# Performance work log

Measured on AMD Instinct MI355X. Metric: run time of the kernel, lower is better.

## Reference

```python
import jax, jax.numpy as jnp
import numpy as np

TOP_K = 2


def setup_inputs() -> dict:
    key = jax.random.key(0)
    k0, k1, k2, k3 = jax.random.split(key, 4)
    T, H, E, I = 512, 2048, 16, 1024  # tokens, hidden, experts, intermediate
    return {
        "hidden_states": jax.random.normal(k0, (T, H), jnp.float32),
        "router_weight": jax.random.normal(k1, (E, H), jnp.float32) * 0.02,
        "w13": jax.random.normal(k2, (E, H, 2 * I), jnp.float32) * 0.02,  # fused gate+up
        "w2": jax.random.normal(k3, (E, I, H), jnp.float32) * 0.02,        # down proj
    }


def reference(hidden_states, router_weight, w13, w2):
    x = hidden_states                                   # [T, H]
    E = router_weight.shape[0]
    # Router: linear (no bias) -> softmax -> top-k -> renormalize
    logits = x @ router_weight.T                        # [T, E]
    probs = jax.nn.softmax(logits, axis=-1)
    vals, idx = jax.lax.top_k(probs, TOP_K)             # [T, K]
    vals = vals / jnp.sum(vals, axis=-1, keepdims=True)
    # Dense combine weights [T, E]: zero except the top-k experts per token
    cw = jnp.sum(jax.nn.one_hot(idx, E, dtype=x.dtype) * vals[..., None], axis=1)
    # Scan over experts; each expert runs a SwiGLU MLP over all tokens,
    # scaled by its (mostly-zero) combine weight. Keeps peak memory at [T, I].
    def body(acc, params):
        w13_e, w2_e, cw_e = params                      # [H,2I], [I,H], [T]
        g, u = jnp.split(x @ w13_e, 2, axis=-1)         # [T, I] each
        acc = acc + cw_e[:, None] * ((jax.nn.silu(g) * u) @ w2_e)
        return acc, None
    out, _ = jax.lax.scan(body, jnp.zeros_like(x), (w13, w2, cw.T))
    return out
```

## Files before the change

### kernel.cpp

```cpp
#include <hip/hip_runtime.h>

#define T_TOK 512
#define HID   2048
#define NEXP  16
#define IDIM  1024
#define KC    64

typedef __attribute__((ext_vector_type(8))) short bf16x8;
typedef __attribute__((ext_vector_type(4))) float f32x4;
typedef __attribute__((ext_vector_type(4))) float float4v;

__device__ __forceinline__ unsigned short f2bf(float f) {
    union { float f; unsigned u; } v; v.f = f;
    return (unsigned short)((v.u + 0x7FFFu + ((v.u >> 16) & 1u)) >> 16);
}

__device__ __forceinline__ unsigned pack2(float lo, float hi) {
    return (unsigned)f2bf(lo) | ((unsigned)f2bf(hi) << 16);
}

__device__ __forceinline__ bf16x8 pack8(const float* s) {
    bf16x8 r;
#pragma unroll
    for (int i = 0; i < 8; ++i) r[i] = (short)f2bf(s[i]);
    return r;
}

__global__ __launch_bounds__(256) void router_kernel(
    const float* __restrict__ x, const float* __restrict__ rw,
    int* __restrict__ cnt, int* __restrict__ tok,
    int* __restrict__ rowid, float* __restrict__ wt,
    unsigned short* __restrict__ xb)
{
    int t = blockIdx.x;
    int tid = threadIdx.x;
    const float* xr = x + (size_t)t * HID;

    {
        int c = tid * 8;
        float4v a = *(const float4v*)(xr + c);
        float4v b = *(const float4v*)(xr + c + 4);
        float tmp[8];
#pragma unroll
        for (int i = 0; i < 4; ++i) { tmp[i] = a[i]; tmp[4 + i] = b[i]; }
        *(bf16x8*)(xb + (size_t)t * HID + c) = pack8(tmp);
    }

    float acc[NEXP];
#pragma unroll
    for (int e = 0; e < NEXP; ++e) acc[e] = 0.f;

    for (int k = tid; k < HID; k += 256) {
        float xv = xr[k];
#pragma unroll
        for (int e = 0; e < NEXP; ++e) acc[e] += xv * rw[e * HID + k];
    }

    __shared__ float red[4][NEXP];
    int lane = tid & 63, wv = tid >> 6;
#pragma unroll
    for (int e = 0; e < NEXP; ++e) {
        float v = acc[e];
#pragma unroll
        for (int off = 32; off > 0; off >>= 1) v += __shfl_down(v, off);
        if (lane == 0) red[wv][e] = v;
    }
    __syncthreads();

    if (tid == 0) {
        float l[NEXP];
        float mx = -1e30f;
#pragma unroll
        for (int e = 0; e < NEXP; ++e) {
            l[e] = red[0][e] + red[1][e] + red[2][e] + red[3][e];
            mx = fmaxf(mx, l[e]);
        }
        float s = 0.f;
#pragma unroll
        for (int e = 0; e < NEXP; ++e) { l[e] = __expf(l[e] - mx); s += l[e]; }
        float inv_s = 1.f / s;
        int i0 = 0; float v0 = -1.f;
        int i1 = 0; float v1 = -2.f;
#pragma unroll
        for (int e = 0; e < NEXP; ++e) {
            float p = l[e] * inv_s;
            if (p > v0)      { v1 = v0; i1 = i0; v0 = p; i0 = e; }
            else if (p > v1) { v1 = p; i1 = e; }
        }
        float inv = 1.f / (v0 + v1);
        int p0 = atomicAdd(&cnt[i0], 1);
        tok[i0 * T_TOK + p0] = t; rowid[i0 * T_TOK + p0] = 2 * t;     wt[i0 * T_TOK + p0] = v0 * inv;
        int p1 = atomicAdd(&cnt[i1], 1);
        tok[i1 * T_TOK + p1] = t; rowid[i1 * T_TOK + p1] = 2 * t + 1; wt[i1 * T_TOK + p1] = v1 * inv;
    }
}

#define LOADW(buf, kk_, stride_) { \
    buf[0] = *(const float4v*)(wsrc + (size_t)((kk_) + kg * 2)     * (stride_)); \
    buf[1] = *(const float4v*)(wsrc + (size_t)((kk_) + kg * 2 + 1) * (stride_)); }

#define STOREW(buf) { _Pragma("unroll") \
    for (int j2 = 0; j2 < 4; ++j2) { \
        int colw = cg * 4 + j2; \
        *(unsigned*)((char*)Ws + ((colw * 128 + kg * 4) ^ ((colw & 7) << 4))) = \
            pack2(buf[0][j2], buf[1][j2]); } }

#define LOADX(buf, kk_) { \
    buf[0] = *(const bf16x8*)(xsrc + (kk_)); \
    buf[1] = *(const bf16x8*)(xsrc + (kk_) + 8); }

#define STOREX(buf) { \
    *(bf16x8*)((char*)Xs + ((xrow * 128 + xq * 32)      ^ xswz)) = buf[0]; \
    *(bf16x8*)((char*)Xs + ((xrow * 128 + xq * 32 + 16) ^ xswz)) = buf[1]; }

__global__ __launch_bounds__(512, 4) void gemm1_kernel(
    const unsigned short* __restrict__ xb, const float* __restrict__ w13,
    const int* __restrict__ cnt, const int* __restrict__ tok,
    const int* __restrict__ rowid, const float* __restrict__ wt,
    unsigned short* __restrict__ h)
{
    int bid = blockIdx.x;
    int e  = bid >> 5;
    int c0 = (bid & 31) * 32;
    int n = cnt[e];
    int tid = threadIdx.x;

    __shared__ __align__(16) short Xs[128 * KC];
    __shared__ __align__(16) short Ws[64 * KC];
    __shared__ int   tks[128];
    __shared__ int   rws[128];
    __shared__ float wts[128];

    const float* wbase = w13 + (size_t)e * HID * (2 * IDIM);

    int cg = tid & 15, kg = tid >> 4;
    const float* wsrc = wbase + ((cg < 8) ? (c0 + cg * 4)
                                          : (IDIM + c0 + (cg - 8) * 4));
    int xrow = tid >> 2, xq = tid & 3;
    int xswz = (xrow & 7) << 4;

    int wave = tid >> 6, lane = tid & 63;
    int lr = lane & 15, lh = lane >> 4;
    int swzA = (lr & 7) << 4;

    for (int t0 = 0; t0 < n; t0 += 128) {
        int nt = min(128, n - t0);
        __syncthreads();
        if (tid < 128) {
            int idx = t0 + min(tid, nt - 1);
            tks[tid] = tok[e * T_TOK + idx];
            rws[tid] = rowid[e * T_TOK + idx];
            wts[tid] = wt[e * T_TOK + idx];
        }
        __syncthreads();

        const unsigned short* xsrc = xb + (size_t)tks[xrow] * HID + xq * 16;

        f32x4 accG[2], accU[2];
#pragma unroll
        for (int i = 0; i < 2; ++i) { accG[i] = (f32x4)0.f; accU[i] = (f32x4)0.f; }

        float4v wbufA[2], wbufB[2];
        bf16x8 xbufA[2], xbufB[2];
        LOADW(wbufA, 0, 2 * IDIM); LOADX(xbufA, 0);

#define G1_MFMA() { \
        if (wave * 16 < nt) { _Pragma("unroll") \
            for (int s = 0; s < 2; ++s) { \
                int kb = (s * 32 + lh * 8) * 2; \
                bf16x8 a = *(const bf16x8*)((char*)Xs + (((wave * 16 + lr) * 128 + kb) ^ swzA)); \
                _Pragma("unroll") for (int cf = 0; cf < 2; ++cf) { \
                    int colg = cf * 16 + lr; \
                    bf16x8 bg = *(const bf16x8*)((char*)Ws + ((colg * 128 + kb) ^ swzA)); \
                    accG[cf] = __builtin_amdgcn_mfma_f32_16x16x32_bf16(a, bg, accG[cf], 0, 0, 0); \
                    bf16x8 bu = *(const bf16x8*)((char*)Ws + (((32 + colg) * 128 + kb) ^ swzA)); \
                    accU[cf] = __builtin_amdgcn_mfma_f32_16x16x32_bf16(a, bu, accU[cf], 0, 0, 0); \
                } \
            } \
        } }

        for (int kk = 0; kk < HID; kk += 2 * KC) {
            LOADW(wbufB, kk + KC, 2 * IDIM); LOADX(xbufB, kk + KC);
            STOREW(wbufA); STOREX(xbufA);
            __syncthreads();
            G1_MFMA();
            __syncthreads();
            if (kk + 2 * KC < HID) { LOADW(wbufA, kk + 2 * KC, 2 * IDIM); LOADX(xbufA, kk + 2 * KC); }
            STOREW(wbufB); STOREX(xbufB);
            __syncthreads();
            G1_MFMA();
            __syncthreads();
        }

#pragma unroll
        for (int cf = 0; cf < 2; ++cf)
#pragma unroll
            for (int r = 0; r < 4; ++r) {
                int row = wave * 16 + lh * 4 + r;
                if (row < nt) {
                    float g = accG[cf][r], u = accU[cf][r];
                    float sg = g / (1.f + __expf(-g));
                    float v = wts[row] * sg * u;
                    h[(size_t)rws[row] * IDIM + c0 + cf * 16 + lr] = f2bf(v);
                }
            }
    }
}

__global__ __launch_bounds__(512, 4) void gemm2_kernel(
    const unsigned short* __restrict__ h, const float* __restrict__ w2,
    const int* __restrict__ cnt, const int* __restrict__ tok,
    const int* __restrict__ rowid,
    float* __restrict__ out)
{
    int bid = blockIdx.x;
    int e  = bid >> 5;
    int c0 = (bid & 31) * 64;
    int n = cnt[e];
    int tid = threadIdx.x;

    __shared__ __align__(16) short Xs[128 * KC];
    __shared__ __align__(16) short Ws[64 * KC];
    __shared__ int   tks[128];
    __shared__ int   rws[128];

    const float* wbase = w2 + (size_t)e * IDIM * HID;

    int cg = tid & 15, kg = tid >> 4;
    const float* wsrc = wbase + c0 + cg * 4;
    int xrow = tid >> 2, xq = tid & 3;
    int xswz = (xrow & 7) << 4;

    int wave = tid >> 6, lane = tid & 63;
    int lr = lane & 15, lh = lane >> 4;
    int swzA = (lr & 7) << 4;

    for (int t0 = 0; t0 < n; t0 += 128) {
        int nt = min(128, n - t0);
        __syncthreads();
        if (tid < 128) {
            int idx = t0 + min(tid, nt - 1);
            tks[tid] = tok[e * T_TOK + idx];
            rws[tid] = rowid[e * T_TOK + idx];
        }
        __syncthreads();

        const unsigned short* xsrc = h + (size_t)rws[xrow] * IDIM + xq * 16;

        f32x4 acc[4];
#pragma unroll
        for (int i = 0; i < 4; ++i) acc[i] = (f32x4)0.f;

        float4v wbufA[2], wbufB[2];
        bf16x8 xbufA[2], xbufB[2];
        LOADW(wbufA, 0, HID); LOADX(xbufA, 0);

#define G2_MFMA() { \
        if (wave * 16 < nt) { _Pragma("unroll") \
            for (int s = 0; s < 2; ++s) { \
                int kb = (s * 32 + lh * 8) * 2; \
                bf16x8 a = *(const bf16x8*)((char*)Xs + (((wave * 16 + lr) * 128 + kb) ^ swzA)); \
                _Pragma("unroll") for (int cf = 0; cf < 4; ++cf) { \
                    int col = cf * 16 + lr; \
                    bf16x8 b = *(const bf16x8*)((char*)Ws + ((col * 128 + kb) ^ swzA)); \
                    acc[cf] = __builtin_amdgcn_mfma_f32_16x16x32_bf16(a, b, acc[cf], 0, 0, 0); \
                } \
            } \
        } }

        for (int kk = 0; kk < IDIM; kk += 2 * KC) {
            LOADW(wbufB, kk + KC, HID); LOADX(xbufB, kk + KC);
            STOREW(wbufA); STOREX(xbufA);
            __syncthreads();
            G2_MFMA();
            __syncthreads();
            if (kk + 2 * KC < IDIM) { LOADW(wbufA, kk + 2 * KC, HID); LOADX(xbufA, kk + 2 * KC); }
            STOREW(wbufB); STOREX(xbufB);
            __syncthreads();
            G2_MFMA();
            __syncthreads();
        }

#pragma unroll
        for (int cf = 0; cf < 4; ++cf)
#pragma unroll
            for (int r = 0; r < 4; ++r) {
                int row = wave * 16 + lh * 4 + r;
                if (row < nt)
                    atomicAdd(&out[(size_t)tks[row] * HID + c0 + cf * 16 + lr], acc[cf][r]);
            }
    }
}

extern "C" void kernel_launch(void* const* d_in, const int* in_sizes, int n_in,
                              void* d_out, int out_size, void* d_ws, size_t ws_size,
                              hipStream_t stream) {
    const float* x   = (const float*)d_in[0];
    const float* rw  = (const float*)d_in[1];
    const float* w13 = (const float*)d_in[2];
    const float* w2  = (const float*)d_in[3];
    float* out = (float*)d_out;

    int* cnt   = (int*)d_ws;
    int* tok   = cnt + 64;
    int* rowid = tok + NEXP * T_TOK;
    float* wt  = (float*)(rowid + NEXP * T_TOK);
    unsigned short* h  = (unsigned short*)((char*)d_ws + 131072);
    unsigned short* xb = (unsigned short*)((char*)d_ws + 131072 + 2097152);

    hipMemsetAsync(out, 0, (size_t)T_TOK * HID * sizeof(float), stream);
    hipMemsetAsync(cnt, 0, 64 * sizeof(int), stream);

    router_kernel<<<T_TOK, 256, 0, stream>>>(x, rw, cnt, tok, rowid, wt, xb);
    gemm1_kernel<<<512, 512, 0, stream>>>(xb, w13, cnt, tok, rowid, wt, h);
    gemm2_kernel<<<512, 512, 0, stream>>>(h, w2, cnt, tok, rowid, out);
}
```

Before: 133.2 us.

## Double-buffer LDS tiles to halve barriers in both MoE GEMM kernels

Both grouped GEMM kernels now keep two LDS buffers for the X and W tiles. The next tile is written into the alternate buffer while MFMAs read the current one, so each K-step needs one barrier instead of two. The aim is less barrier stall and better overlap of the LDS stores with compute. In exchange, LDS use per block doubles (about 48KB), which may cut the number of resident blocks below the launch-bounds target of 4.

```diff
diff --git a/kernel.cpp b/kernel.cpp
--- a/kernel.cpp
+++ b/kernel.cpp
@@ -99,19 +99,19 @@
     buf[0] = *(const float4v*)(wsrc + (size_t)((kk_) + kg * 2)     * (stride_)); \
     buf[1] = *(const float4v*)(wsrc + (size_t)((kk_) + kg * 2 + 1) * (stride_)); }
 
-#define STOREW(buf) { _Pragma("unroll") \
+#define STOREW(buf, Wd) { _Pragma("unroll") \
     for (int j2 = 0; j2 < 4; ++j2) { \
         int colw = cg * 4 + j2; \
-        *(unsigned*)((char*)Ws + ((colw * 128 + kg * 4) ^ ((colw & 7) << 4))) = \
+        *(unsigned*)((char*)(Wd) + ((colw * 128 + kg * 4) ^ ((colw & 7) << 4))) = \
             pack2(buf[0][j2], buf[1][j2]); } }
 
 #define LOADX(buf, kk_) { \
     buf[0] = *(const bf16x8*)(xsrc + (kk_)); \
     buf[1] = *(const bf16x8*)(xsrc + (kk_) + 8); }
 
-#define STOREX(buf) { \
-    *(bf16x8*)((char*)Xs + ((xrow * 128 + xq * 32)      ^ xswz)) = buf[0]; \
-    *(bf16x8*)((char*)Xs + ((xrow * 128 + xq * 32 + 16) ^ xswz)) = buf[1]; }
+#define STOREX(buf, Xd) { \
+    *(bf16x8*)((char*)(Xd) + ((xrow * 128 + xq * 32)      ^ xswz)) = buf[0]; \
+    *(bf16x8*)((char*)(Xd) + ((xrow * 128 + xq * 32 + 16) ^ xswz)) = buf[1]; }
 
 __global__ __launch_bounds__(512, 4) void gemm1_kernel(
     const unsigned short* __restrict__ xb, const float* __restrict__ w13,
@@ -125,8 +125,8 @@
     int n = cnt[e];
     int tid = threadIdx.x;
 
-    __shared__ __align__(16) short Xs[128 * KC];
-    __shared__ __align__(16) short Ws[64 * KC];
+    __shared__ __align__(16) short Xs[2][128 * KC];
+    __shared__ __align__(16) short Ws[2][64 * KC];
     __shared__ int   tks[128];
     __shared__ int   rws[128];
     __shared__ float wts[128];
@@ -143,6 +143,18 @@
     int lr = lane & 15, lh = lane >> 4;
     int swzA = (lr & 7) << 4;
 
+#define G1_MFMA(Xd, Wd) { if (wave * 16 < nt) { _Pragma("unroll") \
+    for (int s = 0; s < 2; ++s) { \
+        int kb = (s * 32 + lh * 8) * 2; \
+        bf16x8 a = *(const bf16x8*)((char*)(Xd) + (((wave * 16 + lr) * 128 + kb) ^ swzA)); \
+        _Pragma("unroll") for (int cf = 0; cf < 2; ++cf) { \
+            int colg = cf * 16 + lr; \
+            bf16x8 bg = *(const bf16x8*)((char*)(Wd) + ((colg * 128 + kb) ^ swzA)); \
+            accG[cf] = __builtin_amdgcn_mfma_f32_16x16x32_bf16(a, bg, accG[cf], 0, 0, 0); \
+            bf16x8 bu = *(const bf16x8*)((char*)(Wd) + (((32 + colg) * 128 + kb) ^ swzA)); \
+            accU[cf] = __builtin_amdgcn_mfma_f32_16x16x32_bf16(a, bu, accU[cf], 0, 0, 0); \
+        } } } }
+
     for (int t0 = 0; t0 < n; t0 += 128) {
         int nt = min(128, n - t0);
         __syncthreads();
@@ -160,35 +172,22 @@
 #pragma unroll
         for (int i = 0; i < 2; ++i) { accG[i] = (f32x4)0.f; accU[i] = (f32x4)0.f; }
 
-        float4v wbufA[2], wbufB[2];
-        bf16x8 xbufA[2], xbufB[2];
-        LOADW(wbufA, 0, 2 * IDIM); LOADX(xbufA, 0);
-
-#define G1_MFMA() { \
-        if (wave * 16 < nt) { _Pragma("unroll") \
-            for (int s = 0; s < 2; ++s) { \
-                int kb = (s * 32 + lh * 8) * 2; \
-                bf16x8 a = *(const bf16x8*)((char*)Xs + (((wave * 16 + lr) * 128 + kb) ^ swzA)); \
-                _Pragma("unroll") for (int cf = 0; cf < 2; ++cf) { \
-                    int colg = cf * 16 + lr; \
-                    bf16x8 bg = *(const bf16x8*)((char*)Ws + ((colg * 128 + kb) ^ swzA)); \
-                    accG[cf] = __builtin_amdgcn_mfma_f32_16x16x32_bf16(a, bg, accG[cf], 0, 0, 0); \
-                    bf16x8 bu = *(const bf16x8*)((char*)Ws + (((32 + colg) * 128 + kb) ^ swzA)); \
-                    accU[cf] = __builtin_amdgcn_mfma_f32_16x16x32_bf16(a, bu, accU[cf], 0, 0, 0); \
-                } \
-            } \
-        } }
-
-        for (int kk = 0; kk < HID; kk += 2 * KC) {
-            LOADW(wbufB, kk + KC, 2 * IDIM); LOADX(xbufB, kk + KC);
-            STOREW(wbufA); STOREX(xbufA);
+        float4v rWa[2], rWb[2];
+        bf16x8 rXa[2], rXb[2];
+        LOADW(rWa, 0, 2 * IDIM);  LOADX(rXa, 0);
+        LOADW(rWb, KC, 2 * IDIM); LOADX(rXb, KC);
+        STOREW(rWa, Ws[0]); STOREX(rXa, Xs[0]);
+        __syncthreads();
+
+        for (int p = 0; p < HID / KC; p += 2) {
+            int kf0 = (p + 2) * KC, kf1 = (p + 3) * KC;
+            if (kf0 < HID) { LOADW(rWa, kf0, 2 * IDIM); LOADX(rXa, kf0); }
+            G1_MFMA(Xs[0], Ws[0]);
+            STOREW(rWb, Ws[1]); STOREX(rXb, Xs[1]);
             __syncthreads();
-            G1_MFMA();
-            __syncthreads();
-            if (kk + 2 * KC < HID) { LOADW(wbufA, kk + 2 * KC, 2 * IDIM); LOADX(xbufA, kk + 2 * KC); }
-            STOREW(wbufB); STOREX(xbufB);
-            __syncthreads();
-            G1_MFMA();
+            if (kf1 < HID) { LOADW(rWb, kf1, 2 * IDIM); LOADX(rXb, kf1); }
+            G1_MFMA(Xs[1], Ws[1]);
+            if (kf0 < HID) { STOREW(rWa, Ws[0]); STOREX(rXa, Xs[0]); }
             __syncthreads();
         }
 
@@ -219,8 +218,8 @@
     int n = cnt[e];
     int tid = threadIdx.x;
 
-    __shared__ __align__(16) short Xs[128 * KC];
-    __shared__ __align__(16) short Ws[64 * KC];
+    __shared__ __align__(16) short Xs[2][128 * KC];
+    __shared__ __align__(16) short Ws[2][64 * KC];
     __shared__ int   tks[128];
     __shared__ int   rws[128];
 
@@ -235,6 +234,16 @@
     int lr = lane & 15, lh = lane >> 4;
     int swzA = (lr & 7) << 4;
 
+#define G2_MFMA(Xd, Wd) { if (wave * 16 < nt) { _Pragma("unroll") \
+    for (int s = 0; s < 2; ++s) { \
+        int kb = (s * 32 + lh * 8) * 2; \
+        bf16x8 a = *(const bf16x8*)((char*)(Xd) + (((wave * 16 + lr) * 128 + kb) ^ swzA)); \
+        _Pragma("unroll") for (int cf = 0; cf < 4; ++cf) { \
+            int col = cf * 16 + lr; \
+            bf16x8 b = *(const bf16x8*)((char*)(Wd) + ((col * 128 + kb) ^ swzA)); \
+            acc[cf] = __builtin_amdgcn_mfma_f32_16x16x32_bf16(a, b, acc[cf], 0, 0, 0); \
+        } } } }
+
     for (int t0 = 0; t0 < n; t0 += 128) {
         int nt = min(128, n - t0);
         __syncthreads();
@@ -251,33 +260,22 @@
 #pragma unroll
         for (int i = 0; i < 4; ++i) acc[i] = (f32x4)0.f;
 
-        float4v wbufA[2], wbufB[2];
-        bf16x8 xbufA[2], xbufB[2];
-        LOADW(wbufA, 0, HID); LOADX(xbufA, 0);
-
-#define G2_MFMA() { \
-        if (wave * 16 < nt) { _Pragma("unroll") \
-            for (int s = 0; s < 2; ++s) { \
-                int kb = (s * 32 + lh * 8) * 2; \
-                bf16x8 a = *(const bf16x8*)((char*)Xs + (((wave * 16 + lr) * 128 + kb) ^ swzA)); \
-                _Pragma("unroll") for (int cf = 0; cf < 4; ++cf) { \
-                    int col = cf * 16 + lr; \
-                    bf16x8 b = *(const bf16x8*)((char*)Ws + ((col * 128 + kb) ^ swzA)); \
-                    acc[cf] = __builtin_amdgcn_mfma_f32_16x16x32_bf16(a, b, acc[cf], 0, 0, 0); \
-                } \
-            } \
-        } }
-
-        for (int kk = 0; kk < IDIM; kk += 2 * KC) {
-            LOADW(wbufB, kk + KC, HID); LOADX(xbufB, kk + KC);
-            STOREW(wbufA); STOREX(xbufA);
+        float4v rWa[2], rWb[2];
+        bf16x8 rXa[2], rXb[2];
+        LOADW(rWa, 0, HID);  LOADX(rXa, 0);
+        LOADW(rWb, KC, HID); LOADX(rXb, KC);
+        STOREW(rWa, Ws[0]); STOREX(rXa, Xs[0]);
+        __syncthreads();
+
+        for (int p = 0; p < IDIM / KC; p += 2) {
+            int kf0 = (p + 2) * KC, kf1 = (p + 3) * KC;
+            if (kf0 < IDIM) { LOADW(rWa, kf0, HID); LOADX(rXa, kf0); }
+            G2_MFMA(Xs[0], Ws[0]);
+            STOREW(rWb, Ws[1]); STOREX(rXb, Xs[1]);
             __syncthreads();
-            G2_MFMA();
-            __syncthreads();
-            if (kk + 2 * KC < IDIM) { LOADW(wbufA, kk + 2 * KC, HID); LOADX(xbufA, kk + 2 * KC); }
-            STOREW(wbufB); STOREX(xbufB);
-            __syncthreads();
-            G2_MFMA();
+            if (kf1 < IDIM) { LOADW(rWb, kf1, HID); LOADX(rXb, kf1); }
+            G2_MFMA(Xs[1], Ws[1]);
+            if (kf0 < IDIM) { STOREW(rWa, Ws[0]); STOREX(rXa, Xs[0]); }
             __syncthreads();
         }
 
```

Measured after the change: 132.9 us. Within noise of the previous version (-0.2%).
